# Optimization experiments

Measured on AMD Instinct MI355X. Metric: run time of the kernel, lower is better.

Reference implementation:

```python
import math
import jax, jax.numpy as jnp
import numpy as np

B, T, C, H = 2, 2048, 1024, 16  # batch, seq, embed, heads; head_dim = C//H = 64

def setup_inputs() -> dict:
    key = jax.random.key(0)
    k1, k2, k3 = jax.random.split(key, 3)
    x = jax.random.normal(k1, (B, T, C), dtype=jnp.float32)
    w_qkv = jax.random.normal(k2, (C, 3 * C), dtype=jnp.float32) * 0.02
    b_qkv = jnp.zeros((3 * C,), dtype=jnp.float32)
    w_proj = jax.random.normal(k3, (C, C), dtype=jnp.float32) * (0.02 / math.sqrt(2 * 24))
    b_proj = jnp.zeros((C,), dtype=jnp.float32)
    return {"x": x, "w_qkv": w_qkv, "b_qkv": b_qkv, "w_proj": w_proj, "b_proj": b_proj}

def reference(x, w_qkv, b_qkv, w_proj, b_proj):
    b, t, c = x.shape
    h = H
    qkv = x @ w_qkv + b_qkv  # [b, t, 3c]
    q, k, v = jnp.split(qkv, 3, axis=-1)
    # [b, t, c] -> [b, h, t, d]
    def heads(z):
        return z.reshape(b, t, h, c // h).transpose(0, 2, 1, 3)
    q, k, v = heads(q), heads(k), heads(v)
    # NOTE: source scales by sqrt(c) (full embed dim), not sqrt(head_dim)
    att = jnp.einsum("bhqd,bhkd->bhqk", q, k) / math.sqrt(c)
    # causal mask: -inf above diagonal
    mask = jnp.triu(jnp.full((t, t), -jnp.inf, dtype=att.dtype), k=1)
    att = att + mask
    att = jax.nn.softmax(att, axis=-1)
    out = jnp.einsum("bhqk,bhkd->bhqd", att, v)  # [b, h, t, d]
    out = out.transpose(0, 2, 1, 3).reshape(b, t, c)
    return out @ w_proj + b_proj
```

## Files before the change

kernel.cpp:

```cpp
#include <hip/hip_runtime.h>
#include <math.h>

#define BSZ 2
#define TSEQ 2048
#define CEMB 1024
#define NHEAD 16
#define HDIM 64

typedef float f32x4 __attribute__((ext_vector_type(4)));
typedef short bf16x8 __attribute__((ext_vector_type(8)));

typedef __attribute__((address_space(3))) char lds_char;
typedef __attribute__((address_space(1))) const char gbl_char;

__device__ __forceinline__ void g2l16(const void* g, void* l) {
    __builtin_amdgcn_global_load_lds((const gbl_char*)g, (lds_char*)l, 16, 0, 0);
}

__device__ __forceinline__ unsigned short f2bf(float x) {
    unsigned u = __float_as_uint(x);
    unsigned r = ((u >> 16) & 1u) + 0x7fffu;
    return (unsigned short)((u + r) >> 16);
}

__global__ __launch_bounds__(256) void conv_f32_bf16(
    const float* __restrict__ in, unsigned short* __restrict__ out)
{
    size_t i = ((size_t)blockIdx.x * 256 + threadIdx.x) * 8;
    float4 a = *(const float4*)(in + i);
    float4 b = *(const float4*)(in + i + 4);
    union { unsigned short u[8]; uint4 v; } pk;
    pk.u[0] = f2bf(a.x); pk.u[1] = f2bf(a.y); pk.u[2] = f2bf(a.z); pk.u[3] = f2bf(a.w);
    pk.u[4] = f2bf(b.x); pk.u[5] = f2bf(b.y); pk.u[6] = f2bf(b.z); pk.u[7] = f2bf(b.w);
    *(uint4*)(out + i) = pk.v;
}

__global__ __launch_bounds__(256) void conv_transpose_bf16(
    const float* __restrict__ w, unsigned short* __restrict__ wT, int K, int N)
{
    __shared__ float t[32][33];
    const int n0 = blockIdx.x * 32, k0 = blockIdx.y * 32;
    const int tx = threadIdx.x & 31, ty = threadIdx.x >> 5;
    #pragma unroll
    for (int i = 0; i < 4; ++i)
        t[ty + i * 8][tx] = w[(size_t)(k0 + ty + i * 8) * N + n0 + tx];
    __syncthreads();
    #pragma unroll
    for (int i = 0; i < 4; ++i) {
        int r = ty + i * 8;
        wT[(size_t)(n0 + r) * K + k0 + tx] = f2bf(t[tx][r]);
    }
}

template <int EPI>
__global__ __launch_bounds__(256) void gemm_mfma(
    const unsigned short* __restrict__ A, const unsigned short* __restrict__ BT,
    const float* __restrict__ bias,
    unsigned short* __restrict__ qo, unsigned short* __restrict__ ko,
    unsigned short* __restrict__ vo, float* __restrict__ fo,
    int M, int N, int K)
{
    __shared__ __align__(16) char sA[128 * 64 * 2];
    __shared__ __align__(16) char sB[128 * 64 * 2];

    const int tid = threadIdx.x;
    const int lane = tid & 63;
    const int wid = tid >> 6;
    const int wm = wid >> 1, wn = wid & 1;
    const int row0 = blockIdx.y * 128;
    const int col0 = blockIdx.x * 128;

    f32x4 acc[4][4] = {};

    for (int k0 = 0; k0 < K; k0 += 64) {
        __syncthreads();
        #pragma unroll
        for (int i = 0; i < 4; ++i) {
            int cid = i * 256 + tid;
            int row = cid >> 3, c2 = cid & 7;
            g2l16(&A[(size_t)(row0 + row) * K + k0 + ((c2 ^ (row & 7)) << 3)],
                  sA + ((i * 256 + (tid & 192)) << 4));
        }
        #pragma unroll
        for (int i = 0; i < 4; ++i) {
            int cid = i * 256 + tid;
            int row = cid >> 3, c2 = cid & 7;
            g2l16(&BT[(size_t)(col0 + row) * K + k0 + ((c2 ^ (row & 7)) << 3)],
                  sB + ((i * 256 + (tid & 192)) << 4));
        }
        __syncthreads();

        #pragma unroll
        for (int ks = 0; ks < 2; ++ks) {
            bf16x8 af[4], bf[4];
            #pragma unroll
            for (int mi = 0; mi < 4; ++mi) {
                int row = wm * 64 + mi * 16 + (lane & 15);
                int ch = ((lane >> 4) + 4 * ks) ^ (row & 7);
                af[mi] = *(const bf16x8*)(sA + row * 128 + (ch << 4));
            }
            #pragma unroll
            for (int ni = 0; ni < 4; ++ni) {
                int row = wn * 64 + ni * 16 + (lane & 15);
                int ch = ((lane >> 4) + 4 * ks) ^ (row & 7);
                bf[ni] = *(const bf16x8*)(sB + row * 128 + (ch << 4));
            }
            #pragma unroll
            for (int mi = 0; mi < 4; ++mi)
                #pragma unroll
                for (int ni = 0; ni < 4; ++ni)
                    acc[mi][ni] = __builtin_amdgcn_mfma_f32_16x16x32_bf16(
                        af[mi], bf[ni], acc[mi][ni], 0, 0, 0);
        }
    }

    #pragma unroll
    for (int mi = 0; mi < 4; ++mi) {
        const int rg = row0 + wm * 64 + mi * 16 + (lane >> 4) * 4;
        #pragma unroll
        for (int ni = 0; ni < 4; ++ni) {
            const int cg = col0 + wn * 64 + ni * 16 + (lane & 15);
            const float bv = bias[cg];
            if (EPI == 1) {
                #pragma unroll
                for (int r = 0; r < 4; ++r)
                    fo[(size_t)(rg + r) * N + cg] = acc[mi][ni][r] + bv;
            } else {
                const int region = col0 >> 10;
                if (region < 2) {
                    unsigned short* dst = region ? ko : qo;
                    const int nn = cg - (region << 10);
                    #pragma unroll
                    for (int r = 0; r < 4; ++r)
                        dst[(size_t)(rg + r) * CEMB + nn] = f2bf(acc[mi][ni][r] + bv);
                } else {
                    const int nloc = cg - 2048;
                    const int h = nloc >> 6, d = nloc & 63;
                    const int b = rg >> 11, t = rg & 2047;
                    ushort4 pk;
                    pk.x = f2bf(acc[mi][ni][0] + bv);
                    pk.y = f2bf(acc[mi][ni][1] + bv);
                    pk.z = f2bf(acc[mi][ni][2] + bv);
                    pk.w = f2bf(acc[mi][ni][3] + bv);
                    *(ushort4*)&vo[(((size_t)b * NHEAD + h) * HDIM + d) * TSEQ + t] = pk;
                }
            }
        }
    }
}

__global__ __launch_bounds__(256) void flash_mfma(
    const unsigned short* __restrict__ qb, const unsigned short* __restrict__ kb,
    const unsigned short* __restrict__ vt, unsigned short* __restrict__ ob)
{
    const int u = blockIdx.x >> 5;
    const int bh = blockIdx.x & 31;
    const int qt = (u & 1) ? (31 - (u >> 1)) : (u >> 1);
    const int b = bh >> 4, h = bh & 15;
    const int q0 = qt * 64;

    __shared__ __align__(16) char sQ[8192];
    __shared__ __align__(16) char sK[8192];
    __shared__ __align__(16) char sV[8192];
    __shared__ __align__(16) char sP[8192];

    const int tid = threadIdx.x;
    const int lane = tid & 63;
    const int wid = tid >> 6;

    #pragma unroll
    for (int i = 0; i < 2; ++i) {
        int cid = i * 256 + tid;
        int row = cid >> 3, c2 = cid & 7;
        g2l16(&qb[(size_t)(b * TSEQ + q0 + row) * CEMB + h * HDIM + ((c2 ^ (row & 7)) << 3)],
              sQ + ((i * 256 + (tid & 192)) << 4));
    }

    f32x4 o[4] = {};
    float m[4], l[4];
    #pragma unroll
    for (int r = 0; r < 4; ++r) { m[r] = -INFINITY; l[r] = 0.f; }
    const float scale = 0.03125f;

    for (int kt = 0; kt <= qt; ++kt) {
        const int k0 = kt * 64;
        __syncthreads();
        #pragma unroll
        for (int i = 0; i < 2; ++i) {
            int cid = i * 256 + tid;
            int row = cid >> 3, c2 = cid & 7;
            g2l16(&kb[(size_t)(b * TSEQ + k0 + row) * CEMB + h * HDIM + ((c2 ^ (row & 7)) << 3)],
                  sK + ((i * 256 + (tid & 192)) << 4));
        }
        #pragma unroll
        for (int i = 0; i < 2; ++i) {
            int cid = i * 256 + tid;
            int row = cid >> 3, c2 = cid & 7;
            g2l16(&vt[(((size_t)b * NHEAD + h) * HDIM + row) * TSEQ + k0 + ((c2 ^ (row & 7)) << 3)],
                  sV + ((i * 256 + (tid & 192)) << 4));
        }
        __syncthreads();

        bf16x8 qf[2];
        #pragma unroll
        for (int ks = 0; ks < 2; ++ks) {
            int row = wid * 16 + (lane & 15);
            int ch = ((lane >> 4) + 4 * ks) ^ (row & 7);
            qf[ks] = *(const bf16x8*)(sQ + row * 128 + (ch << 4));
        }
        f32x4 s[4] = {};
        #pragma unroll
        for (int ni = 0; ni < 4; ++ni) {
            #pragma unroll
            for (int ks = 0; ks < 2; ++ks) {
                int row = ni * 16 + (lane & 15);
                int ch = ((lane >> 4) + 4 * ks) ^ (row & 7);
                bf16x8 kf = *(const bf16x8*)(sK + row * 128 + (ch << 4));
                s[ni] = __builtin_amdgcn_mfma_f32_16x16x32_bf16(qf[ks], kf, s[ni], 0, 0, 0);
            }
        }

        #pragma unroll
        for (int ni = 0; ni < 4; ++ni)
            #pragma unroll
            for (int r = 0; r < 4; ++r)
                s[ni][r] *= scale;
        if (kt == qt) {
            #pragma unroll
            for (int ni = 0; ni < 4; ++ni) {
                const int colg = k0 + ni * 16 + (lane & 15);
                #pragma unroll
                for (int r = 0; r < 4; ++r) {
                    const int rowg = q0 + wid * 16 + (lane >> 4) * 4 + r;
                    if (colg > rowg) s[ni][r] = -INFINITY;
                }
            }
        }

        #pragma unroll
        for (int r = 0; r < 4; ++r) {
            float v = fmaxf(fmaxf(s[0][r], s[1][r]), fmaxf(s[2][r], s[3][r]));
            v = fmaxf(v, __shfl_xor(v, 1));
            v = fmaxf(v, __shfl_xor(v, 2));
            v = fmaxf(v, __shfl_xor(v, 4));
            v = fmaxf(v, __shfl_xor(v, 8));
            const float mnew = fmaxf(m[r], v);
            const float sc = __expf(m[r] - mnew);
            m[r] = mnew;
            float ps = 0.f;
            #pragma unroll
            for (int ni = 0; ni < 4; ++ni) {
                const float p = __expf(s[ni][r] - mnew);
                s[ni][r] = p;
                ps += p;
            }
            ps += __shfl_xor(ps, 1);
            ps += __shfl_xor(ps, 2);
            ps += __shfl_xor(ps, 4);
            ps += __shfl_xor(ps, 8);
            l[r] = l[r] * sc + ps;
            #pragma unroll
            for (int ni = 0; ni < 4; ++ni)
                o[ni][r] *= sc;
        }

        #pragma unroll
        for (int ni = 0; ni < 4; ++ni) {
            #pragma unroll
            for (int r = 0; r < 4; ++r) {
                const int prow = wid * 16 + (lane >> 4) * 4 + r;
                const int pcol = ni * 16 + (lane & 15);
                const int byte = prow * 128 + ((((pcol >> 3) ^ (prow & 7))) << 4) + ((pcol & 7) << 1);
                *(unsigned short*)(sP + byte) = f2bf(s[ni][r]);
            }
        }
        asm volatile("s_waitcnt lgkmcnt(0)" ::: "memory");

        bf16x8 pf[2];
        #pragma unroll
        for (int ks = 0; ks < 2; ++ks) {
            int row = wid * 16 + (lane & 15);
            int ch = ((lane >> 4) + 4 * ks) ^ (row & 7);
            pf[ks] = *(const bf16x8*)(sP + row * 128 + (ch << 4));
        }
        #pragma unroll
        for (int ni = 0; ni < 4; ++ni) {
            #pragma unroll
            for (int ks = 0; ks < 2; ++ks) {
                int row = ni * 16 + (lane & 15);
                int ch = ((lane >> 4) + 4 * ks) ^ (row & 7);
                bf16x8 vf = *(const bf16x8*)(sV + row * 128 + (ch << 4));
                o[ni] = __builtin_amdgcn_mfma_f32_16x16x32_bf16(pf[ks], vf, o[ni], 0, 0, 0);
            }
        }
    }

    float linv[4];
    #pragma unroll
    for (int r = 0; r < 4; ++r) linv[r] = 1.f / l[r];
    #pragma unroll
    for (int ni = 0; ni < 4; ++ni) {
        #pragma unroll
        for (int r = 0; r < 4; ++r) {
            const int rowt = q0 + wid * 16 + (lane >> 4) * 4 + r;
            const int col = h * HDIM + ni * 16 + (lane & 15);
            ob[(size_t)(b * TSEQ + rowt) * CEMB + col] = f2bf(o[ni][r] * linv[r]);
        }
    }
}

extern "C" void kernel_launch(void* const* d_in, const int* in_sizes, int n_in,
                              void* d_out, int out_size, void* d_ws, size_t ws_size,
                              hipStream_t stream)
{
    (void)in_sizes; (void)n_in; (void)out_size; (void)ws_size;

    const float* x      = (const float*)d_in[0];
    const float* w_qkv  = (const float*)d_in[1];
    const float* b_qkv  = (const float*)d_in[2];
    const float* w_proj = (const float*)d_in[3];
    const float* b_proj = (const float*)d_in[4];
    float* out = (float*)d_out;

    const int M = BSZ * TSEQ;
    unsigned short* xb     = (unsigned short*)d_ws;
    unsigned short* wqkvT  = xb     + (size_t)M * CEMB;
    unsigned short* wprojT = wqkvT  + (size_t)3 * CEMB * CEMB;
    unsigned short* qbuf   = wprojT + (size_t)CEMB * CEMB;
    unsigned short* kbuf   = qbuf   + (size_t)M * CEMB;
    unsigned short* vbuf   = kbuf   + (size_t)M * CEMB;
    unsigned short* attb   = vbuf   + (size_t)M * CEMB;

    conv_f32_bf16<<<dim3((M * CEMB) / 2048), 256, 0, stream>>>(x, xb);
    conv_transpose_bf16<<<dim3(3 * CEMB / 32, CEMB / 32), 256, 0, stream>>>(
        w_qkv, wqkvT, CEMB, 3 * CEMB);
    conv_transpose_bf16<<<dim3(CEMB / 32, CEMB / 32), 256, 0, stream>>>(
        w_proj, wprojT, CEMB, CEMB);

    gemm_mfma<0><<<dim3(3 * CEMB / 128, M / 128), 256, 0, stream>>>(
        xb, wqkvT, b_qkv, qbuf, kbuf, vbuf, nullptr, M, 3 * CEMB, CEMB);

    flash_mfma<<<dim3(32 * 32), 256, 0, stream>>>(qbuf, kbuf, vbuf, attb);

    gemm_mfma<1><<<dim3(CEMB / 128, M / 128), 256, 0, stream>>>(
        attb, wprojT, b_proj, nullptr, nullptr, nullptr, out, M, CEMB, CEMB);
}
```

Before: 211.5 us.

## Transpose MFMA operands in flash attention for per-lane rows with lazy rescaling

Swaps the MFMA A/B operands so each lane holds a single query row's scores. This turns row max/sum reductions into two cross-group shuffles instead of four per element. It folds log2e into the scale and switches to exp2f, and skips the output rescale unless the running max grows by more than a threshold (lazy rescaling). P is written to LDS as packed 8-byte stores instead of scalar 2-byte stores, and the output goes through LDS for coalesced 16-byte global writes. The costs are an extra pair of block syncs at the end and a wave-uniform branch in the softmax.

```diff
diff --git a/kernel.cpp b/kernel.cpp
--- a/kernel.cpp
+++ b/kernel.cpp
@@ -167,6 +167,9 @@
     const int tid = threadIdx.x;
     const int lane = tid & 63;
     const int wid = tid >> 6;
+    const int g = lane >> 4;
+    const int lr = lane & 15;
+    const int q7 = lr & 7;
 
     #pragma unroll
     for (int i = 0; i < 2; ++i) {
@@ -177,10 +180,8 @@
     }
 
     f32x4 o[4] = {};
-    float m[4], l[4];
-    #pragma unroll
-    for (int r = 0; r < 4; ++r) { m[r] = -INFINITY; l[r] = 0.f; }
-    const float scale = 0.03125f;
+    float mrow = -INFINITY, lrow = 0.f;
+    const float c = 0.0450744431f;
 
     for (int kt = 0; kt <= qt; ++kt) {
         const int k0 = kt * 64;
@@ -204,8 +205,8 @@
         bf16x8 qf[2];
         #pragma unroll
         for (int ks = 0; ks < 2; ++ks) {
-            int row = wid * 16 + (lane & 15);
-            int ch = ((lane >> 4) + 4 * ks) ^ (row & 7);
+            int row = wid * 16 + lr;
+            int ch = (g + 4 * ks) ^ q7;
             qf[ks] = *(const bf16x8*)(sQ + row * 128 + (ch << 4));
         }
         f32x4 s[4] = {};
@@ -213,10 +214,10 @@
         for (int ni = 0; ni < 4; ++ni) {
             #pragma unroll
             for (int ks = 0; ks < 2; ++ks) {
-                int row = ni * 16 + (lane & 15);
-                int ch = ((lane >> 4) + 4 * ks) ^ (row & 7);
+                int row = ni * 16 + lr;
+                int ch = (g + 4 * ks) ^ q7;
                 bf16x8 kf = *(const bf16x8*)(sK + row * 128 + (ch << 4));
-                s[ni] = __builtin_amdgcn_mfma_f32_16x16x32_bf16(qf[ks], kf, s[ni], 0, 0, 0);
+                s[ni] = __builtin_amdgcn_mfma_f32_16x16x32_bf16(kf, qf[ks], s[ni], 0, 0, 0);
             }
         }
 
@@ -224,88 +225,97 @@
         for (int ni = 0; ni < 4; ++ni)
             #pragma unroll
             for (int r = 0; r < 4; ++r)
-                s[ni][r] *= scale;
+                s[ni][r] *= c;
+        const int qrow_g = q0 + wid * 16 + lr;
         if (kt == qt) {
             #pragma unroll
-            for (int ni = 0; ni < 4; ++ni) {
-                const int colg = k0 + ni * 16 + (lane & 15);
+            for (int ni = 0; ni < 4; ++ni)
                 #pragma unroll
-                for (int r = 0; r < 4; ++r) {
-                    const int rowg = q0 + wid * 16 + (lane >> 4) * 4 + r;
-                    if (colg > rowg) s[ni][r] = -INFINITY;
-                }
-            }
-        }
-
+                for (int r = 0; r < 4; ++r)
+                    if (k0 + ni * 16 + g * 4 + r > qrow_g) s[ni][r] = -INFINITY;
+        }
+
+        f32x4 m01, m23;
         #pragma unroll
         for (int r = 0; r < 4; ++r) {
-            float v = fmaxf(fmaxf(s[0][r], s[1][r]), fmaxf(s[2][r], s[3][r]));
-            v = fmaxf(v, __shfl_xor(v, 1));
-            v = fmaxf(v, __shfl_xor(v, 2));
-            v = fmaxf(v, __shfl_xor(v, 4));
-            v = fmaxf(v, __shfl_xor(v, 8));
-            const float mnew = fmaxf(m[r], v);
-            const float sc = __expf(m[r] - mnew);
-            m[r] = mnew;
-            float ps = 0.f;
-            #pragma unroll
-            for (int ni = 0; ni < 4; ++ni) {
-                const float p = __expf(s[ni][r] - mnew);
-                s[ni][r] = p;
+            m01[r] = fmaxf(s[0][r], s[1][r]);
+            m23[r] = fmaxf(s[2][r], s[3][r]);
+        }
+        float v = fmaxf(fmaxf(fmaxf(m01[0], m23[0]), fmaxf(m01[1], m23[1])),
+                        fmaxf(fmaxf(m01[2], m23[2]), fmaxf(m01[3], m23[3])));
+        v = fmaxf(v, __shfl_xor(v, 16));
+        v = fmaxf(v, __shfl_xor(v, 32));
+
+        if (!__all(v <= mrow + 8.f)) {
+            const float mnew = fmaxf(mrow, v);
+            const float sc = exp2f(mrow - mnew);
+            lrow *= sc;
+            #pragma unroll
+            for (int ni = 0; ni < 4; ++ni)
+                #pragma unroll
+                for (int r = 0; r < 4; ++r)
+                    o[ni][r] *= sc;
+            mrow = mnew;
+        }
+
+        float ps = 0.f;
+        #pragma unroll
+        for (int ni = 0; ni < 4; ++ni) {
+            ushort4 pk;
+            #pragma unroll
+            for (int r = 0; r < 4; ++r) {
+                const float p = exp2f(s[ni][r] - mrow);
                 ps += p;
-            }
-            ps += __shfl_xor(ps, 1);
-            ps += __shfl_xor(ps, 2);
-            ps += __shfl_xor(ps, 4);
-            ps += __shfl_xor(ps, 8);
-            l[r] = l[r] * sc + ps;
-            #pragma unroll
-            for (int ni = 0; ni < 4; ++ni)
-                o[ni][r] *= sc;
-        }
-
+                ((unsigned short*)&pk)[r] = f2bf(p);
+            }
+            const int ch = (2 * ni + (g >> 1)) ^ q7;
+            *(uint2*)(sP + (wid * 16 + lr) * 128 + (ch << 4) + ((g & 1) << 3)) =
+                *(const uint2*)&pk;
+        }
+        ps += __shfl_xor(ps, 16);
+        ps += __shfl_xor(ps, 32);
+        lrow += ps;
+
+        asm volatile("s_waitcnt lgkmcnt(0)" ::: "memory");
+
+        bf16x8 pf[2];
+        #pragma unroll
+        for (int ks = 0; ks < 2; ++ks) {
+            int ch = (g + 4 * ks) ^ q7;
+            pf[ks] = *(const bf16x8*)(sP + (wid * 16 + lr) * 128 + (ch << 4));
+        }
         #pragma unroll
         for (int ni = 0; ni < 4; ++ni) {
             #pragma unroll
-            for (int r = 0; r < 4; ++r) {
-                const int prow = wid * 16 + (lane >> 4) * 4 + r;
-                const int pcol = ni * 16 + (lane & 15);
-                const int byte = prow * 128 + ((((pcol >> 3) ^ (prow & 7))) << 4) + ((pcol & 7) << 1);
-                *(unsigned short*)(sP + byte) = f2bf(s[ni][r]);
-            }
-        }
-        asm volatile("s_waitcnt lgkmcnt(0)" ::: "memory");
-
-        bf16x8 pf[2];
-        #pragma unroll
-        for (int ks = 0; ks < 2; ++ks) {
-            int row = wid * 16 + (lane & 15);
-            int ch = ((lane >> 4) + 4 * ks) ^ (row & 7);
-            pf[ks] = *(const bf16x8*)(sP + row * 128 + (ch << 4));
-        }
-        #pragma unroll
-        for (int ni = 0; ni < 4; ++ni) {
-            #pragma unroll
             for (int ks = 0; ks < 2; ++ks) {
-                int row = ni * 16 + (lane & 15);
-                int ch = ((lane >> 4) + 4 * ks) ^ (row & 7);
+                int row = ni * 16 + lr;
+                int ch = (g + 4 * ks) ^ q7;
                 bf16x8 vf = *(const bf16x8*)(sV + row * 128 + (ch << 4));
-                o[ni] = __builtin_amdgcn_mfma_f32_16x16x32_bf16(pf[ks], vf, o[ni], 0, 0, 0);
-            }
-        }
-    }
-
-    float linv[4];
-    #pragma unroll
-    for (int r = 0; r < 4; ++r) linv[r] = 1.f / l[r];
+                o[ni] = __builtin_amdgcn_mfma_f32_16x16x32_bf16(vf, pf[ks], o[ni], 0, 0, 0);
+            }
+        }
+    }
+
+    const float linv = 1.f / lrow;
+    __syncthreads();
     #pragma unroll
     for (int ni = 0; ni < 4; ++ni) {
-        #pragma unroll
-        for (int r = 0; r < 4; ++r) {
-            const int rowt = q0 + wid * 16 + (lane >> 4) * 4 + r;
-            const int col = h * HDIM + ni * 16 + (lane & 15);
-            ob[(size_t)(b * TSEQ + rowt) * CEMB + col] = f2bf(o[ni][r] * linv[r]);
-        }
+        ushort4 pk;
+        #pragma unroll
+        for (int r = 0; r < 4; ++r)
+            ((unsigned short*)&pk)[r] = f2bf(o[ni][r] * linv);
+        const int ch = (2 * ni + (g >> 1)) ^ q7;
+        *(uint2*)(sP + (wid * 16 + lr) * 128 + (ch << 4) + ((g & 1) << 3)) =
+            *(const uint2*)&pk;
+    }
+    __syncthreads();
+    #pragma unroll
+    for (int i = 0; i < 2; ++i) {
+        const int cid = i * 256 + tid;
+        const int row = cid >> 3;
+        const int ch = cid & 7;
+        uint4 val = *(const uint4*)(sP + row * 128 + ((ch ^ (row & 7)) << 4));
+        *(uint4*)&ob[(size_t)(b * TSEQ + q0 + row) * CEMB + h * HDIM + ch * 8] = val;
     }
 }
 
```

After: 196.3 us. -7.2%, faster.
